# Kernel tuning notes

Hardware: AMD Instinct MI355X
Metric: run time of the kernel (lower is better)

Reference implementation:

```python
import jax, jax.numpy as jnp
import numpy as np

# QuadraticConv2DTranspose reconstruction:
#   1) bed-of-nails upsample by stride s (pixels at i*s, zeros elsewhere), padded by k-1
#      so a VALID conv yields output H*s x W*s ('same' transpose-conv geometry)
#   2) per-(pixel, in_channel) flattened k*k patch p (K=k*k values)
#   3) quadratic features: upper-triangular outer products p_i*p_j (K*(K+1)/2 terms),
#      plus linear terms p (K) and a bias term 1  -> L = 55 for k=3
#   4) contract features against flat_kernel [1,1,L,Cin,Cout]

KH = 3            # kernel height/width
STRIDE = 2
KK = KH * KH      # flattened patch size per channel = 9
L = KK * (KK + 1) // 2 + KK + 1  # 45 quad + 9 linear + 1 bias = 55
B, H, W, CIN, COUT = 8, 32, 32, 64, 64


def setup_inputs() -> dict:
    key = jax.random.key(0)
    k1, k2 = jax.random.split(key)
    x = jax.random.normal(k1, (B, H, W, CIN), dtype=jnp.float32)
    flat_kernel = jax.random.normal(k2, (1, 1, L, CIN, COUT), dtype=jnp.float32) * 0.02
    return {"x": x, "flat_kernel": flat_kernel}


def _quadratic_conv_transpose(x, flat_kernel):
    b, h, w, c = x.shape
    k, s = KH, STRIDE
    pad = k - 1
    pb = pad // 2
    # bed-of-nails upsampling into a pre-padded buffer: [B, H*s + k-1, W*s + k-1, C]
    up = jnp.zeros((b, h * s + pad, w * s + pad, c), dtype=x.dtype)
    up = up.at[:, pb:pb + h * s:s, pb:pb + w * s:s, :].set(x)
    # im2col: [B, Ho, Wo, C*K] with feature dim ordered (C, kh, kw)
    patches = jax.lax.conv_general_dilated_patches(
        up, (k, k), (1, 1), 'VALID',
        dimension_numbers=('NHWC', 'HWIO', 'NHWC'))
    ho, wo = h * s, w * s
    p = patches.reshape(b, ho, wo, c, KK)  # per-channel flattened patch
    iu, ju = np.triu_indices(KK)           # 45 upper-triangular index pairs
    quad = p[..., iu] * p[..., ju]         # [B,Ho,Wo,C,45]
    ones = jnp.ones(p.shape[:-1] + (1,), dtype=p.dtype)
    feat = jnp.concatenate([quad, p, ones], axis=-1)  # [B,Ho,Wo,C,L]
    # contract over (L, Cin) against kernel [L,Cin,Cout]
    return jnp.einsum('bhwcl,lco->bhwo', feat, flat_kernel[0, 0])


def reference(x, flat_kernel):
    return _quadratic_conv_transpose(x, flat_kernel)
```

## Files before the change

kernel.cpp:

```cpp
#include <hip/hip_runtime.h>
#include <stdint.h>


typedef __attribute__((ext_vector_type(8))) short short8;
typedef __attribute__((ext_vector_type(4))) short short4v;
typedef __attribute__((ext_vector_type(4))) float floatx4;

__device__ __forceinline__ short f2bf(float f) {
  union { float f; uint32_t u; } v{f};
  uint32_t u = v.u;
  u += 0x7fffu + ((u >> 16) & 1u);
  return (short)(u >> 16);
}

template <int CLS> struct CI;
template <> struct CI<0> {
  static constexpr int NV = 1, NF = 2;
  static constexpr int L[NF] = {30, 49};
  static constexpr int A[NF] = {0, 0};
  static constexpr int Bb[NF] = {0, 1};
  static constexpr int DY[NV] = {0};
  static constexpr int DX[NV] = {0};
};
template <> struct CI<1> {
  static constexpr int NV = 2, NF = 5;
  static constexpr int L[NF] = {24, 26, 35, 48, 50};
  static constexpr int A[NF] = {0, 0, 1, 0, 1};
  static constexpr int Bb[NF] = {0, 1, 1, 2, 2};
  static constexpr int DY[NV] = {0, 0};
  static constexpr int DX[NV] = {0, 1};
};
template <> struct CI<2> {
  static constexpr int NV = 2, NF = 5;
  static constexpr int L[NF] = {9, 15, 42, 46, 52};
  static constexpr int A[NF] = {0, 0, 1, 0, 1};
  static constexpr int Bb[NF] = {0, 1, 1, 2, 2};
  static constexpr int DY[NV] = {0, 1};
  static constexpr int DX[NV] = {0, 0};
};
template <> struct CI<3> {
  static constexpr int NV = 4, NF = 14;
  static constexpr int L[NF] = {0, 2, 6, 8, 17, 21, 23, 39, 41, 44, 45, 47, 51, 53};
  static constexpr int A[NF] = {0, 0, 0, 0, 1, 1, 1, 2, 2, 3, 0, 1, 2, 3};
  static constexpr int Bb[NF] = {0, 1, 2, 3, 1, 2, 3, 2, 3, 3, 4, 4, 4, 4};
  static constexpr int DY[NV] = {0, 0, 1, 1};
  static constexpr int DX[NV] = {0, 1, 0, 1};
};

__global__ __launch_bounds__(256) void prep_w(const float* __restrict__ kern,
                                              short* __restrict__ wt,
                                              float* __restrict__ bias) {
  __shared__ float s[64][65];
  const int l = blockIdx.x;
  const int tid = threadIdx.x;
  for (int i = tid; i < 4096; i += 256)
    s[i >> 6][i & 63] = kern[(l << 12) + i];
  __syncthreads();
  if (l == 54 && tid < 64) {
    float a = 0.f;
    for (int c = 0; c < 64; ++c) a += s[c][tid];
    bias[tid] = a;
  }
  for (int i = tid; i < 1024; i += 256) {
    const int n = i >> 4, c4 = (i & 15) * 4;
    short4v v;
    v[0] = f2bf(s[c4 + 0][n]);
    v[1] = f2bf(s[c4 + 1][n]);
    v[2] = f2bf(s[c4 + 2][n]);
    v[3] = f2bf(s[c4 + 3][n]);
    *(short4v*)&wt[((l << 6) + n) * 64 + c4] = v;
  }
}

template <int CLS>
__device__ __forceinline__ void body(const float* __restrict__ x,
                                     const short* __restrict__ wt,
                                     const float* __restrict__ bias,
                                     float* __restrict__ out, int b, int hi0,
                                     int wi0, float (&sX)[45][68]) {
  using I = CI<CLS>;
  constexpr int NV = I::NV, NF = I::NF;
  const int tid = threadIdx.x;
  const int wave = tid >> 6, lane = tid & 63;
  const int quad = lane >> 4, l16 = lane & 15;
  const int mb = (wave & 1) * 16;
  const int nh = (wave >> 1) * 32;
  const int m = mb + l16;
  const int ph = m >> 3, pw = m & 7;
  const int c8 = quad * 8;

  for (int i = tid; i < 720; i += 256) {
    const int pos = i >> 4, c4 = (i & 15) * 4;
    const int hr = hi0 + pos / 9, wc = wi0 + pos % 9;
    float4 v = make_float4(0.f, 0.f, 0.f, 0.f);
    if (hr < 32 && wc < 32)
      v = *(const float4*)&x[(((b * 32) + hr) * 32 + wc) * 64 + c4];
    *(float4*)&sX[pos][c4] = v;
  }

  floatx4 acc[2];
#pragma unroll
  for (int nt = 0; nt < 2; ++nt) {
    const float bv = bias[nh + nt * 16 + l16];
    acc[nt] = floatx4{bv, bv, bv, bv};
  }

  __syncthreads();

  float vpl[NV][16];
#pragma unroll
  for (int j = 0; j < NV; ++j) {
    const int pa = (ph + I::DY[j]) * 9 + (pw + I::DX[j]);
    *(float4*)&vpl[j][0] = *(const float4*)&sX[pa][c8];
    *(float4*)&vpl[j][4] = *(const float4*)&sX[pa][c8 + 4];
    *(float4*)&vpl[j][8] = *(const float4*)&sX[pa][32 + c8];
    *(float4*)&vpl[j][12] = *(const float4*)&sX[pa][32 + c8 + 4];
  }

#pragma unroll
  for (int chalf = 0; chalf < 2; ++chalf) {
#pragma unroll
    for (int f = 0; f < NF; ++f) {
      const short* wr = wt + (I::L[f] * 64) * 64 + chalf * 32 + c8;
      const short8 b0 = *(const short8*)&wr[(nh + l16) * 64];
      const short8 b1 = *(const short8*)&wr[(nh + 16 + l16) * 64];
      short8 af;
#pragma unroll
      for (int j = 0; j < 8; ++j) {
        const float va = vpl[I::A[f]][chalf * 8 + j];
        const float v = (I::Bb[f] == NV) ? va : va * vpl[I::Bb[f]][chalf * 8 + j];
        af[j] = f2bf(v);
      }
      acc[0] = __builtin_amdgcn_mfma_f32_16x16x32_bf16(af, b0, acc[0], 0, 0, 0);
      acc[1] = __builtin_amdgcn_mfma_f32_16x16x32_bf16(af, b1, acc[1], 0, 0, 0);
    }
  }

  constexpr int rh = CLS >> 1, rw = CLS & 1;
#pragma unroll
  for (int nt = 0; nt < 2; ++nt) {
    const int n = nh + nt * 16 + l16;
#pragma unroll
    for (int r = 0; r < 4; ++r) {
      const int mm = mb + quad * 4 + r;
      const int hi = hi0 + (mm >> 3), wi = wi0 + (mm & 7);
      const int ho = 2 * hi + rh, wo = 2 * wi + rw;
      out[(((b * 64) + ho) * 64 + wo) * 64 + n] = acc[nt][r];
    }
  }
}

__global__ __launch_bounds__(256, 4) void qct_main(const float* __restrict__ x,
                                                   const short* __restrict__ wt,
                                                   const float* __restrict__ bias,
                                                   float* __restrict__ out) {
  __shared__ float sX[45][68];
  const int bid = blockIdx.x;
  int cls, blk;
  if (bid < 256)      { cls = 3; blk = bid; }
  else if (bid < 512) { cls = 1; blk = bid - 256; }
  else if (bid < 768) { cls = 2; blk = bid - 512; }
  else                { cls = 0; blk = bid - 768; }
  const int b = blk >> 5, tile = blk & 31;
  const int hi0 = (tile >> 2) * 4;
  const int wi0 = (tile & 3) * 8;
  switch (cls) {
    case 0: body<0>(x, wt, bias, out, b, hi0, wi0, sX); break;
    case 1: body<1>(x, wt, bias, out, b, hi0, wi0, sX); break;
    case 2: body<2>(x, wt, bias, out, b, hi0, wi0, sX); break;
    case 3: body<3>(x, wt, bias, out, b, hi0, wi0, sX); break;
  }
}

extern "C" void kernel_launch(void* const* d_in, const int* in_sizes, int n_in,
                              void* d_out, int out_size, void* d_ws,
                              size_t ws_size, hipStream_t stream) {
  const float* x = (const float*)d_in[0];
  const float* kern = (const float*)d_in[1];
  float* out = (float*)d_out;
  short* wt = (short*)d_ws;
  float* bias = (float*)((char*)d_ws + 55 * 64 * 64 * 2);

  prep_w<<<55, 256, 0, stream>>>(kern, wt, bias);
  qct_main<<<1024, 256, 0, stream>>>(x, wt, bias, out);
}
```

Before: 75.00 us.

## Merge four output parity classes into one block sharing patch products

Replaces the four per-parity-class block types (1024 blocks of 256 threads) with 256 blocks of 512 threads. Each block computes all four output parity classes, so the input tile is staged once, and the 14 bf16 product and linear fragments are formed once and reused across 26 MFMAs feeding four accumulators. It also switches to a packed bf16 conversion via perm, with simplified rounding. This removes redundant staging and feature computation and per-class load imbalance, in exchange for fewer blocks, more registers per thread and constant-memory index tables.

```diff
diff --git a/kernel.cpp b/kernel.cpp
--- a/kernel.cpp
+++ b/kernel.cpp
@@ -13,39 +13,19 @@
   return (short)(u >> 16);
 }
 
-template <int CLS> struct CI;
-template <> struct CI<0> {
-  static constexpr int NV = 1, NF = 2;
-  static constexpr int L[NF] = {30, 49};
-  static constexpr int A[NF] = {0, 0};
-  static constexpr int Bb[NF] = {0, 1};
-  static constexpr int DY[NV] = {0};
-  static constexpr int DX[NV] = {0};
-};
-template <> struct CI<1> {
-  static constexpr int NV = 2, NF = 5;
-  static constexpr int L[NF] = {24, 26, 35, 48, 50};
-  static constexpr int A[NF] = {0, 0, 1, 0, 1};
-  static constexpr int Bb[NF] = {0, 1, 1, 2, 2};
-  static constexpr int DY[NV] = {0, 0};
-  static constexpr int DX[NV] = {0, 1};
-};
-template <> struct CI<2> {
-  static constexpr int NV = 2, NF = 5;
-  static constexpr int L[NF] = {9, 15, 42, 46, 52};
-  static constexpr int A[NF] = {0, 0, 1, 0, 1};
-  static constexpr int Bb[NF] = {0, 1, 1, 2, 2};
-  static constexpr int DY[NV] = {0, 1};
-  static constexpr int DX[NV] = {0, 0};
-};
-template <> struct CI<3> {
-  static constexpr int NV = 4, NF = 14;
-  static constexpr int L[NF] = {0, 2, 6, 8, 17, 21, 23, 39, 41, 44, 45, 47, 51, 53};
-  static constexpr int A[NF] = {0, 0, 0, 0, 1, 1, 1, 2, 2, 3, 0, 1, 2, 3};
-  static constexpr int Bb[NF] = {0, 1, 2, 3, 1, 2, 3, 2, 3, 3, 4, 4, 4, 4};
-  static constexpr int DY[NV] = {0, 0, 1, 1};
-  static constexpr int DX[NV] = {0, 1, 0, 1};
-};
+__device__ __forceinline__ uint32_t pk2bf(float a, float b) {
+  union { float f; uint32_t u; } x{a}, y{b};
+  return __builtin_amdgcn_perm(y.u + 0x8000u, x.u + 0x8000u, 0x07060302u);
+}
+
+__constant__ __device__ const int cQA[10] = {0, 0, 0, 0, 1, 1, 1, 2, 2, 3};
+__constant__ __device__ const int cQB[10] = {0, 1, 2, 3, 1, 2, 3, 2, 3, 3};
+__constant__ __device__ const int cPP[26] = {0, 0, 0, 0, 1, 1, 2, 2, 3, 4, 4, 5, 6,
+                                             7, 7, 8, 9, 10, 10, 10, 10, 11, 11, 12, 12, 13};
+__constant__ __device__ const int cPC[26] = {0, 1, 2, 3, 1, 3, 2, 3, 3, 1, 3, 3, 3,
+                                             2, 3, 3, 3, 0, 1, 2, 3, 1, 3, 2, 3, 3};
+__constant__ __device__ const int cPL[26] = {30, 24, 9, 0, 26, 2, 15, 6, 8, 35, 17, 21, 23,
+                                             42, 39, 41, 44, 49, 48, 46, 45, 50, 47, 52, 51, 53};
 
 __global__ __launch_bounds__(256) void prep_w(const float* __restrict__ kern,
                                               short* __restrict__ wt,
@@ -72,24 +52,18 @@
   }
 }
 
-template <int CLS>
-__device__ __forceinline__ void body(const float* __restrict__ x,
-                                     const short* __restrict__ wt,
-                                     const float* __restrict__ bias,
-                                     float* __restrict__ out, int b, int hi0,
-                                     int wi0, float (&sX)[45][68]) {
-  using I = CI<CLS>;
-  constexpr int NV = I::NV, NF = I::NF;
+__global__ __launch_bounds__(512, 2) void qct_main(const float* __restrict__ x,
+                                                   const short* __restrict__ wt,
+                                                   const float* __restrict__ bias,
+                                                   float* __restrict__ out) {
+  __shared__ float sX[45][68];
   const int tid = threadIdx.x;
-  const int wave = tid >> 6, lane = tid & 63;
-  const int quad = lane >> 4, l16 = lane & 15;
-  const int mb = (wave & 1) * 16;
-  const int nh = (wave >> 1) * 32;
-  const int m = mb + l16;
-  const int ph = m >> 3, pw = m & 7;
-  const int c8 = quad * 8;
+  const int bid = blockIdx.x;
+  const int b = bid >> 5, tile = bid & 31;
+  const int hi0 = (tile >> 2) * 4;
+  const int wi0 = (tile & 3) * 8;
 
-  for (int i = tid; i < 720; i += 256) {
+  for (int i = tid; i < 720; i += 512) {
     const int pos = i >> 4, c4 = (i & 15) * 4;
     const int hr = hi0 + pos / 9, wc = wi0 + pos % 9;
     float4 v = make_float4(0.f, 0.f, 0.f, 0.f);
@@ -98,77 +72,72 @@
     *(float4*)&sX[pos][c4] = v;
   }
 
-  floatx4 acc[2];
-#pragma unroll
-  for (int nt = 0; nt < 2; ++nt) {
-    const float bv = bias[nh + nt * 16 + l16];
-    acc[nt] = floatx4{bv, bv, bv, bv};
+  const int wave = tid >> 6, lane = tid & 63;
+  const int quad = lane >> 4, l16 = lane & 15;
+  const int mh = wave >> 2;
+  const int nt = wave & 3;
+  const int n = nt * 16 + l16;
+  const int p = mh * 16 + l16;
+  const int ph = p >> 3, pw = p & 7;
+  const int c8 = quad * 8;
+
+  floatx4 acc[4];
+  {
+    const float bv = bias[n];
+    acc[0] = acc[1] = acc[2] = acc[3] = floatx4{bv, bv, bv, bv};
   }
 
   __syncthreads();
 
-  float vpl[NV][16];
 #pragma unroll
-  for (int j = 0; j < NV; ++j) {
-    const int pa = (ph + I::DY[j]) * 9 + (pw + I::DX[j]);
-    *(float4*)&vpl[j][0] = *(const float4*)&sX[pa][c8];
-    *(float4*)&vpl[j][4] = *(const float4*)&sX[pa][c8 + 4];
-    *(float4*)&vpl[j][8] = *(const float4*)&sX[pa][32 + c8];
-    *(float4*)&vpl[j][12] = *(const float4*)&sX[pa][32 + c8 + 4];
+  for (int chalf = 0; chalf < 2; ++chalf) {
+    const int cb = chalf * 32 + c8;
+    float v[4][8];
+#pragma unroll
+    for (int dy = 0; dy < 2; ++dy)
+#pragma unroll
+      for (int dx = 0; dx < 2; ++dx) {
+        const int pa = (ph + dy) * 9 + (pw + dx);
+        *(float4*)&v[dy * 2 + dx][0] = *(const float4*)&sX[pa][cb];
+        *(float4*)&v[dy * 2 + dx][4] = *(const float4*)&sX[pa][cb + 4];
+      }
+    short8 pr[14];
+#pragma unroll
+    for (int q = 0; q < 10; ++q) {
+      union { uint32_t w[4]; short8 s; } u;
+#pragma unroll
+      for (int h = 0; h < 4; ++h)
+        u.w[h] = pk2bf(v[cQA[q]][2 * h] * v[cQB[q]][2 * h],
+                       v[cQA[q]][2 * h + 1] * v[cQB[q]][2 * h + 1]);
+      pr[q] = u.s;
+    }
+#pragma unroll
+    for (int t = 0; t < 4; ++t) {
+      union { uint32_t w[4]; short8 s; } u;
+#pragma unroll
+      for (int h = 0; h < 4; ++h)
+        u.w[h] = pk2bf(v[t][2 * h], v[t][2 * h + 1]);
+      pr[10 + t] = u.s;
+    }
+#pragma unroll
+    for (int s = 0; s < 26; ++s) {
+      const short8 bf =
+          *(const short8*)&wt[((cPL[s] * 64) + n) * 64 + chalf * 32 + c8];
+      acc[cPC[s]] =
+          __builtin_amdgcn_mfma_f32_16x16x32_bf16(pr[cPP[s]], bf, acc[cPC[s]], 0, 0, 0);
+    }
   }
 
 #pragma unroll
-  for (int chalf = 0; chalf < 2; ++chalf) {
-#pragma unroll
-    for (int f = 0; f < NF; ++f) {
-      const short* wr = wt + (I::L[f] * 64) * 64 + chalf * 32 + c8;
-      const short8 b0 = *(const short8*)&wr[(nh + l16) * 64];
-      const short8 b1 = *(const short8*)&wr[(nh + 16 + l16) * 64];
-      short8 af;
-#pragma unroll
-      for (int j = 0; j < 8; ++j) {
-        const float va = vpl[I::A[f]][chalf * 8 + j];
-        const float v = (I::Bb[f] == NV) ? va : va * vpl[I::Bb[f]][chalf * 8 + j];
-        af[j] = f2bf(v);
-      }
-      acc[0] = __builtin_amdgcn_mfma_f32_16x16x32_bf16(af, b0, acc[0], 0, 0, 0);
-      acc[1] = __builtin_amdgcn_mfma_f32_16x16x32_bf16(af, b1, acc[1], 0, 0, 0);
-    }
-  }
-
-  constexpr int rh = CLS >> 1, rw = CLS & 1;
-#pragma unroll
-  for (int nt = 0; nt < 2; ++nt) {
-    const int n = nh + nt * 16 + l16;
+  for (int cls = 0; cls < 4; ++cls) {
+    const int rh = cls >> 1, rw = cls & 1;
 #pragma unroll
     for (int r = 0; r < 4; ++r) {
-      const int mm = mb + quad * 4 + r;
+      const int mm = mh * 16 + quad * 4 + r;
       const int hi = hi0 + (mm >> 3), wi = wi0 + (mm & 7);
       const int ho = 2 * hi + rh, wo = 2 * wi + rw;
-      out[(((b * 64) + ho) * 64 + wo) * 64 + n] = acc[nt][r];
+      out[(((b * 64) + ho) * 64 + wo) * 64 + n] = acc[cls][r];
     }
-  }
-}
-
-__global__ __launch_bounds__(256, 4) void qct_main(const float* __restrict__ x,
-                                                   const short* __restrict__ wt,
-                                                   const float* __restrict__ bias,
-                                                   float* __restrict__ out) {
-  __shared__ float sX[45][68];
-  const int bid = blockIdx.x;
-  int cls, blk;
-  if (bid < 256)      { cls = 3; blk = bid; }
-  else if (bid < 512) { cls = 1; blk = bid - 256; }
-  else if (bid < 768) { cls = 2; blk = bid - 512; }
-  else                { cls = 0; blk = bid - 768; }
-  const int b = blk >> 5, tile = blk & 31;
-  const int hi0 = (tile >> 2) * 4;
-  const int wi0 = (tile & 3) * 8;
-  switch (cls) {
-    case 0: body<0>(x, wt, bias, out, b, hi0, wi0, sX); break;
-    case 1: body<1>(x, wt, bias, out, b, hi0, wi0, sX); break;
-    case 2: body<2>(x, wt, bias, out, b, hi0, wi0, sX); break;
-    case 3: body<3>(x, wt, bias, out, b, hi0, wi0, sX); break;
   }
 }
 
@@ -182,5 +151,5 @@
   float* bias = (float*)((char*)d_ws + 55 * 64 * 64 * 2);
 
   prep_w<<<55, 256, 0, stream>>>(kern, wt, bias);
-  qct_main<<<1024, 256, 0, stream>>>(x, wt, bias, out);
+  qct_main<<<256, 512, 0, stream>>>(x, wt, bias, out);
 }
```

Result: slower. 77.52 us (+3.4%).

## Fuse weight bf16 conversion into main kernel via double-buffered shared memory

Applied to the files above, without the earlier changes.

Drops the separate weight-preparation launch. Each block now reads the fp32 kernel slices it needs, packs them to bf16 into a double-buffered shared-memory tile and reduces the bias itself, with a barrier per feature. The bf16 pack now uses a perm-based round-half-up instead of round-to-nearest-even. This saves a kernel launch and the intermediate workspace round trip, but every block repeats the weight conversion and adds per-feature synchronisation and L2 traffic.

```diff
diff --git a/kernel.cpp b/kernel.cpp
--- a/kernel.cpp
+++ b/kernel.cpp
@@ -3,14 +3,11 @@
 
 
 typedef __attribute__((ext_vector_type(8))) short short8;
-typedef __attribute__((ext_vector_type(4))) short short4v;
 typedef __attribute__((ext_vector_type(4))) float floatx4;
 
-__device__ __forceinline__ short f2bf(float f) {
-  union { float f; uint32_t u; } v{f};
-  uint32_t u = v.u;
-  u += 0x7fffu + ((u >> 16) & 1u);
-  return (short)(u >> 16);
+__device__ __forceinline__ uint32_t pk2bf(float a, float b) {
+  union { float f; uint32_t u; } x{a}, y{b};
+  return __builtin_amdgcn_perm(y.u + 0x8000u, x.u + 0x8000u, 0x07060302u);
 }
 
 template <int CLS> struct CI;
@@ -47,37 +44,13 @@
   static constexpr int DX[NV] = {0, 1, 0, 1};
 };
 
-__global__ __launch_bounds__(256) void prep_w(const float* __restrict__ kern,
-                                              short* __restrict__ wt,
-                                              float* __restrict__ bias) {
-  __shared__ float s[64][65];
-  const int l = blockIdx.x;
-  const int tid = threadIdx.x;
-  for (int i = tid; i < 4096; i += 256)
-    s[i >> 6][i & 63] = kern[(l << 12) + i];
-  __syncthreads();
-  if (l == 54 && tid < 64) {
-    float a = 0.f;
-    for (int c = 0; c < 64; ++c) a += s[c][tid];
-    bias[tid] = a;
-  }
-  for (int i = tid; i < 1024; i += 256) {
-    const int n = i >> 4, c4 = (i & 15) * 4;
-    short4v v;
-    v[0] = f2bf(s[c4 + 0][n]);
-    v[1] = f2bf(s[c4 + 1][n]);
-    v[2] = f2bf(s[c4 + 2][n]);
-    v[3] = f2bf(s[c4 + 3][n]);
-    *(short4v*)&wt[((l << 6) + n) * 64 + c4] = v;
-  }
-}
-
 template <int CLS>
 __device__ __forceinline__ void body(const float* __restrict__ x,
-                                     const short* __restrict__ wt,
-                                     const float* __restrict__ bias,
+                                     const float* __restrict__ kern,
                                      float* __restrict__ out, int b, int hi0,
-                                     int wi0, float (&sX)[45][68]) {
+                                     int wi0, float (&sX)[45][68],
+                                     short (&sB)[2][64][72],
+                                     float (&sbias)[4][64]) {
   using I = CI<CLS>;
   constexpr int NV = I::NV, NF = I::NF;
   const int tid = threadIdx.x;
@@ -88,6 +61,16 @@
   const int m = mb + l16;
   const int ph = m >> 3, pw = m & 7;
   const int c8 = quad * 8;
+  const int sn = lane;
+  const int skb = wave * 16;
+
+  {
+    float s = 0.f;
+    const float* bp = &kern[(54 * 64 + wave * 16) * 64 + sn];
+#pragma unroll
+    for (int c = 0; c < 16; ++c) s += bp[c * 64];
+    sbias[wave][sn] = s;
+  }
 
   for (int i = tid; i < 720; i += 256) {
     const int pos = i >> 4, c4 = (i & 15) * 4;
@@ -97,14 +80,6 @@
       v = *(const float4*)&x[(((b * 32) + hr) * 32 + wc) * 64 + c4];
     *(float4*)&sX[pos][c4] = v;
   }
-
-  floatx4 acc[2];
-#pragma unroll
-  for (int nt = 0; nt < 2; ++nt) {
-    const float bv = bias[nh + nt * 16 + l16];
-    acc[nt] = floatx4{bv, bv, bv, bv};
-  }
-
   __syncthreads();
 
   float vpl[NV][16];
@@ -117,22 +92,49 @@
     *(float4*)&vpl[j][12] = *(const float4*)&sX[pa][32 + c8 + 4];
   }
 
+  floatx4 acc[2];
 #pragma unroll
-  for (int chalf = 0; chalf < 2; ++chalf) {
+  for (int nt = 0; nt < 2; ++nt) {
+    const int n = nh + nt * 16 + l16;
+    const float bv = sbias[0][n] + sbias[1][n] + sbias[2][n] + sbias[3][n];
+    acc[nt] = floatx4{bv, bv, bv, bv};
+  }
+
+#pragma unroll 1
+  for (int f = 0; f < NF; ++f) {
+    short(&B)[64][72] = sB[f & 1];
+    {
+      const float* src = &kern[(I::L[f] * 64 + skb) * 64 + sn];
+      float w[16];
 #pragma unroll
-    for (int f = 0; f < NF; ++f) {
-      const short* wr = wt + (I::L[f] * 64) * 64 + chalf * 32 + c8;
-      const short8 b0 = *(const short8*)&wr[(nh + l16) * 64];
-      const short8 b1 = *(const short8*)&wr[(nh + 16 + l16) * 64];
-      short8 af;
+      for (int j = 0; j < 16; ++j) w[j] = src[j * 64];
+      union { uint32_t d[8]; short8 s[2]; } u;
 #pragma unroll
-      for (int j = 0; j < 8; ++j) {
-        const float va = vpl[I::A[f]][chalf * 8 + j];
-        const float v = (I::Bb[f] == NV) ? va : va * vpl[I::Bb[f]][chalf * 8 + j];
-        af[j] = f2bf(v);
+      for (int h = 0; h < 8; ++h) u.d[h] = pk2bf(w[2 * h], w[2 * h + 1]);
+      *(short8*)&B[sn][skb] = u.s[0];
+      *(short8*)&B[sn][skb + 8] = u.s[1];
+    }
+    __syncthreads();
+    short8 af[2];
+#pragma unroll
+    for (int ch = 0; ch < 2; ++ch) {
+      union { uint32_t d[4]; short8 s; } ua;
+#pragma unroll
+      for (int h = 0; h < 4; ++h) {
+        const int j0 = ch * 8 + 2 * h, j1 = j0 + 1;
+        float a0 = vpl[I::A[f]][j0], a1 = vpl[I::A[f]][j1];
+        if (I::Bb[f] != NV) { a0 *= vpl[I::Bb[f]][j0]; a1 *= vpl[I::Bb[f]][j1]; }
+        ua.d[h] = pk2bf(a0, a1);
       }
-      acc[0] = __builtin_amdgcn_mfma_f32_16x16x32_bf16(af, b0, acc[0], 0, 0, 0);
-      acc[1] = __builtin_amdgcn_mfma_f32_16x16x32_bf16(af, b1, acc[1], 0, 0, 0);
+      af[ch] = ua.s;
+    }
+#pragma unroll
+    for (int nt = 0; nt < 2; ++nt) {
+      const int n = nh + nt * 16 + l16;
+      const short8 b0 = *(const short8*)&B[n][c8];
+      const short8 b1 = *(const short8*)&B[n][32 + c8];
+      acc[nt] = __builtin_amdgcn_mfma_f32_16x16x32_bf16(af[0], b0, acc[nt], 0, 0, 0);
+      acc[nt] = __builtin_amdgcn_mfma_f32_16x16x32_bf16(af[1], b1, acc[nt], 0, 0, 0);
     }
   }
 
@@ -150,11 +152,12 @@
   }
 }
 
-__global__ __launch_bounds__(256, 4) void qct_main(const float* __restrict__ x,
-                                                   const short* __restrict__ wt,
-                                                   const float* __restrict__ bias,
-                                                   float* __restrict__ out) {
+__global__ __launch_bounds__(256) void qct_main(const float* __restrict__ x,
+                                                const float* __restrict__ kern,
+                                                float* __restrict__ out) {
   __shared__ float sX[45][68];
+  __shared__ __align__(16) short sB[2][64][72];
+  __shared__ float sbias[4][64];
   const int bid = blockIdx.x;
   int cls, blk;
   if (bid < 256)      { cls = 3; blk = bid; }
@@ -165,10 +168,10 @@
   const int hi0 = (tile >> 2) * 4;
   const int wi0 = (tile & 3) * 8;
   switch (cls) {
-    case 0: body<0>(x, wt, bias, out, b, hi0, wi0, sX); break;
-    case 1: body<1>(x, wt, bias, out, b, hi0, wi0, sX); break;
-    case 2: body<2>(x, wt, bias, out, b, hi0, wi0, sX); break;
-    case 3: body<3>(x, wt, bias, out, b, hi0, wi0, sX); break;
+    case 0: body<0>(x, kern, out, b, hi0, wi0, sX, sB, sbias); break;
+    case 1: body<1>(x, kern, out, b, hi0, wi0, sX, sB, sbias); break;
+    case 2: body<2>(x, kern, out, b, hi0, wi0, sX, sB, sbias); break;
+    case 3: body<3>(x, kern, out, b, hi0, wi0, sX, sB, sbias); break;
   }
 }
 
@@ -178,9 +181,6 @@
   const float* x = (const float*)d_in[0];
   const float* kern = (const float*)d_in[1];
   float* out = (float*)d_out;
-  short* wt = (short*)d_ws;
-  float* bias = (float*)((char*)d_ws + 55 * 64 * 64 * 2);
-
-  prep_w<<<55, 256, 0, stream>>>(kern, wt, bias);
-  qct_main<<<1024, 256, 0, stream>>>(x, wt, bias, out);
+  (void)d_ws; (void)ws_size;
+  qct_main<<<1024, 256, 0, stream>>>(x, kern, out);
 }
```

After: 101.7 us. +35.6%, slower.
